# Kernel tuning notes

Hardware: AMD Instinct MI355X
Metric: run time of the kernel (lower is better)

## Reference

```python
import jax, jax.numpy as jnp
import numpy as np

B, S, XDIM, YDIM = 64, 1024, 256, 128


def setup_inputs() -> dict:
    key = jax.random.key(0)
    ks = jax.random.split(key, 7)
    q = jax.random.normal(ks[0], (B, S, XDIM), dtype=jnp.float32)
    # Linear weights in torch layout [out, in]; biases [out]
    sc = 1.0 / np.sqrt(XDIM)
    Wq = jax.random.normal(ks[1], (YDIM, XDIM), dtype=jnp.float32) * sc
    Wk = jax.random.normal(ks[2], (YDIM, XDIM), dtype=jnp.float32) * sc
    Wv = jax.random.normal(ks[3], (YDIM, XDIM), dtype=jnp.float32) * sc
    bq = jax.random.normal(ks[4], (YDIM,), dtype=jnp.float32) * sc
    bk = jax.random.normal(ks[5], (YDIM,), dtype=jnp.float32) * sc
    bv = jax.random.normal(ks[6], (YDIM,), dtype=jnp.float32) * sc
    return {"q": q, "Wq": Wq, "bq": bq, "Wk": Wk, "bk": bk, "Wv": Wv, "bv": bv}


def reference(q, Wq, bq, Wk, bk, Wv, bv):
    # Q, K, V projections: [B, S, YDIM]
    Q = jnp.einsum('bsx,yx->bsy', q, Wq) + bq
    K = jnp.einsum('bsx,yx->bsy', q, Wk) + bk
    V = jnp.einsum('bsx,yx->bsy', q, Wv) + bv
    scale = jnp.float32(np.sqrt(YDIM))
    # scores [B, S_q, S_k]; softmax over the QUERY axis (dim=-2), non-standard
    scores = jnp.einsum('bqd,bkd->bqk', Q, K) / scale
    attn = jax.nn.softmax(scores, axis=-2)
    out = jnp.einsum('bqk,bkd->bqd', attn, V)  # [B, S, YDIM]
    # flat=True: max over dim=-2 -> [B, YDIM]
    return jnp.max(out, axis=-2)
```

## Files before the change

### kernel.cpp

```cpp
#include <hip/hip_runtime.h>

typedef __bf16 bf16;
typedef __attribute__((ext_vector_type(8))) __bf16 bf16x8;
typedef __attribute__((ext_vector_type(4))) __bf16 bf16x4;
typedef __attribute__((ext_vector_type(4))) float  f32x4;

static __device__ __forceinline__ f32x4 mfma16(bf16x8 a, bf16x8 b, f32x4 c) {
  return __builtin_amdgcn_mfma_f32_16x16x32_bf16(a, b, c, 0, 0, 0);
}
static __device__ __forceinline__ float fexp2(float x) {
  return __builtin_amdgcn_exp2f(x);
}
static __device__ __forceinline__ float flog2(float x) {
  return __builtin_amdgcn_logf(x);
}

#define EXP_C1 (1.4426950408889634f / 11.313708498984760f)

typedef const __attribute__((address_space(1))) unsigned int gas_u32;
typedef __attribute__((address_space(3))) unsigned int las_u32;
#define GLDS16(gp, lp) __builtin_amdgcn_global_load_lds((gas_u32*)(gp), (las_u32*)(lp), 16, 0, 0)

#define DMA_FENCE() __asm__ volatile("s_waitcnt vmcnt(0)" ::: "memory")


__global__ __launch_bounds__(256) void k_prep(
    const float* __restrict__ Wq, const float* __restrict__ Wk,
    const float* __restrict__ Wv, bf16* __restrict__ Wc)
{
  int id = blockIdx.x * 256 + threadIdx.x;
  int proj = id >> 12, r = id & 4095;
  int g = r >> 7, n = r & 127;
  const float* W = proj == 0 ? Wq : proj == 1 ? Wk : Wv;
  const float sc = (proj == 0) ? EXP_C1 : 1.0f;
  const float4* src = (const float4*)(W + n * 256 + g * 8);
  float4 a = src[0], b = src[1];
  bf16x8 o = { (bf16)(a.x * sc), (bf16)(a.y * sc), (bf16)(a.z * sc), (bf16)(a.w * sc),
               (bf16)(b.x * sc), (bf16)(b.y * sc), (bf16)(b.z * sc), (bf16)(b.w * sc) };
  *(bf16x8*)(Wc + (size_t)proj * 32768 + g * 1024 + n * 8) = o;
}

__global__ __launch_bounds__(256, 4) void k_qkv(
    const float* __restrict__ q, const bf16* __restrict__ Wc,
    const float* __restrict__ bq, const float* __restrict__ bk, const float* __restrict__ bv,
    bf16* __restrict__ Qb, bf16* __restrict__ Kb, bf16* __restrict__ VT)
{
  __shared__ bf16 Al[32 * 520];

  const int tid = threadIdx.x, lane = tid & 63, wave = tid >> 6;
  const int ln = lane & 15, quad = lane >> 4;
  const int wc = wave;
  const int m0 = blockIdx.x * 64;

  {
    const float* src = q + (size_t)m0 * 256;
    for (int it = 0; it < 16; ++it) {
      int f = it * 1024 + tid * 4;
      int r = f >> 8, c = f & 255;
      float4 v = *(const float4*)(src + f);
      bf16x4 o = { (bf16)v.x, (bf16)v.y, (bf16)v.z, (bf16)v.w };
      *(bf16x4*)&Al[(c >> 3) * 520 + r * 8 + (c & 7)] = o;
    }
  }
  __syncthreads();

  const int b = m0 >> 10, st = (m0 & 1023) >> 7, s_off = m0 & 64;
  const size_t tbase = ((size_t)b * 8 + st) * 16384;

  for (int p = 0; p < 3; ++p) {
    const bf16* W = Wc + (size_t)p * 32768;
    const float* bias = p == 0 ? bq : p == 1 ? bk : bv;
    if (p < 2) {
      f32x4 acc[2][4] = {};
      for (int kk = 0; kk < 8; ++kk) {
        int g = kk * 4 + quad;
        bf16x8 ax[4], bw[2];
        for (int t = 0; t < 4; ++t)
          ax[t] = *(const bf16x8*)&Al[g * 520 + (t * 16 + ln) * 8];
        for (int t = 0; t < 2; ++t)
          bw[t] = *(const bf16x8*)(W + g * 1024 + (wc * 32 + t * 16 + ln) * 8);
        for (int i = 0; i < 2; ++i)
          for (int j = 0; j < 4; ++j)
            acc[i][j] = mfma16(bw[i], ax[j], acc[i][j]);
      }
      bf16* dst = (p == 0 ? Qb : Kb) + tbase;
      for (int i = 0; i < 2; ++i) {
        float4 b4 = *(const float4*)&bias[wc * 32 + i * 16 + quad * 4];
        if (p == 0) { b4.x *= EXP_C1; b4.y *= EXP_C1; b4.z *= EXP_C1; b4.w *= EXP_C1; }
        int gd = wc * 4 + i * 2 + (quad >> 1);
        int e0 = (quad & 1) * 4;
        for (int j = 0; j < 4; ++j) {
          int s = s_off + j * 16 + ln;
          bf16x4 o = { (bf16)(acc[i][j][0] + b4.x), (bf16)(acc[i][j][1] + b4.y),
                       (bf16)(acc[i][j][2] + b4.z), (bf16)(acc[i][j][3] + b4.w) };
          *(bf16x4*)&dst[(size_t)gd * 1024 + (size_t)s * 8 + e0] = o;
        }
      }
    } else {
      f32x4 acc[4][2] = {};
      for (int kk = 0; kk < 8; ++kk) {
        int g = kk * 4 + quad;
        bf16x8 ax[4], bw[2];
        for (int t = 0; t < 4; ++t)
          ax[t] = *(const bf16x8*)&Al[g * 520 + (t * 16 + ln) * 8];
        for (int t = 0; t < 2; ++t)
          bw[t] = *(const bf16x8*)(W + g * 1024 + (wc * 32 + t * 16 + ln) * 8);
        for (int i = 0; i < 4; ++i)
          for (int j = 0; j < 2; ++j)
            acc[i][j] = mfma16(ax[i], bw[j], acc[i][j]);
      }
      bf16* dst = VT + tbase;
      for (int j = 0; j < 2; ++j) {
        int d = wc * 32 + j * 16 + ln;
        float bb = bias[d];
        for (int i = 0; i < 4; ++i) {
          int s0 = s_off + i * 16 + quad * 4;
          int G  = (s0 >> 5) * 4 + ((s0 & 15) >> 2);
          int e0 = (s0 & 16) >> 2;
          bf16x4 o = { (bf16)(acc[i][j][0] + bb), (bf16)(acc[i][j][1] + bb),
                       (bf16)(acc[i][j][2] + bb), (bf16)(acc[i][j][3] + bb) };
          *(bf16x4*)&dst[(size_t)G * 1024 + (size_t)d * 8 + e0] = o;
        }
      }
    }
  }
}

__global__ __launch_bounds__(256, 2) void k_stats(
    const bf16* __restrict__ Qb, const bf16* __restrict__ Kb, float* __restrict__ nlg)
{
  __shared__ char Qbuf[2][32768];
  const int b = blockIdx.x, kt = blockIdx.y;
  const int tid = threadIdx.x, lane = tid & 63, wave = tid >> 6;
  const int ln = lane & 15, quad = lane >> 4;

  const bf16* ktile = Kb + ((size_t)b * 8 + kt) * 16384;
  bf16x8 ak[2][4];
  for (int i = 0; i < 2; ++i)
    for (int kk = 0; kk < 4; ++kk)
      ak[i][kk] = *(const bf16x8*)(ktile + (kk * 4 + quad) * 1024 + (wave * 32 + i * 16 + ln) * 8);

  const char* qb_b = (const char*)(Qb + (size_t)b * 8 * 16384);
  for (int c = 0; c < 8; ++c)
    GLDS16(qb_b + (wave * 8 + c) * 1024 + lane * 16, &Qbuf[0][(wave * 8 + c) * 1024]);

  f32x4 csum[2] = {};
  for (int qt = 0; qt < 8; ++qt) {
    DMA_FENCE();
    __syncthreads();
    if (qt < 7)
      for (int c = 0; c < 8; ++c)
        GLDS16(qb_b + (size_t)(qt + 1) * 32768 + (wave * 8 + c) * 1024 + lane * 16,
               &Qbuf[(qt + 1) & 1][(wave * 8 + c) * 1024]);
    const char* Ql = Qbuf[qt & 1];
    for (int jq = 0; jq < 8; ++jq) {
      f32x4 s0 = {}, s1 = {};
      __builtin_amdgcn_s_setprio(1);
      for (int kk = 0; kk < 4; ++kk) {
        bf16x8 bqf = *(const bf16x8*)(Ql + ((kk * 4 + quad) * 2 + (jq >> 2)) * 1024
                                         + ((jq * 16 + ln) & 63) * 16);
        s0 = mfma16(ak[0][kk], bqf, s0);
        s1 = mfma16(ak[1][kk], bqf, s1);
      }
      __builtin_amdgcn_s_setprio(0);
      for (int rr = 0; rr < 4; ++rr) {
        csum[0][rr] += fexp2(s0[rr]);
        csum[1][rr] += fexp2(s1[rr]);
      }
    }
  }
  for (int i = 0; i < 2; ++i)
    for (int rr = 0; rr < 4; ++rr) {
      float v = csum[i][rr];
      v += __shfl_xor(v, 1, 64); v += __shfl_xor(v, 2, 64);
      v += __shfl_xor(v, 4, 64); v += __shfl_xor(v, 8, 64);
      csum[i][rr] = v;
    }
  if (ln == 0) {
    float* dst = nlg + (size_t)b * 1024 + kt * 128 + wave * 32 + quad * 4;
    for (int i = 0; i < 2; ++i)
      for (int rr = 0; rr < 4; ++rr)
        dst[i * 16 + rr] = -flog2(csum[i][rr]);
  }
}

__global__ __launch_bounds__(256, 2) void k_attn(
    const bf16* __restrict__ Qb, const bf16* __restrict__ Kb, const bf16* __restrict__ VT,
    const float* __restrict__ nlg, float* __restrict__ Opart)
{
  __shared__ char buf[2][32768];
  __shared__ float nll[1024];
  __shared__ float redm[4][128];

  const int b = blockIdx.x, qt = blockIdx.y;
  const int tid = threadIdx.x, lane = tid & 63, wave = tid >> 6;
  const int ln = lane & 15, quad = lane >> 4;

  *(float4*)&nll[tid * 4] = *(const float4*)(nlg + (size_t)b * 1024 + tid * 4);

  const bf16* qtile = Qb + ((size_t)b * 8 + qt) * 16384;
  bf16x8 bq_[2][4];
  for (int j = 0; j < 2; ++j)
    for (int kk = 0; kk < 4; ++kk)
      bq_[j][kk] = *(const bf16x8*)(qtile + (kk * 4 + quad) * 1024 + (wave * 32 + j * 16 + ln) * 8);

  const char* kb_b = (const char*)(Kb + (size_t)b * 8 * 16384);
  const char* vt_b = (const char*)(VT + (size_t)b * 8 * 16384);

#define DMA_TILE(t) do {                                                         \
    const char* ksrc = kb_b + (size_t)((t) >> 1) * 32768 + ((t) & 1) * 1024;     \
    const char* vsrc = vt_b + (size_t)((t) >> 1) * 32768 + ((t) & 1) * 16384;    \
    char* d_ = buf[(t) & 1];                                                     \
    for (int c = 0; c < 4; ++c) {                                                \
      int ch = wave * 4 + c;                                                     \
      GLDS16(ksrc + ch * 2048 + lane * 16, d_ + ch * 1024);                      \
      GLDS16(vsrc + (ch >> 1) * 2048 + (ch & 1) * 1024 + lane * 16,              \
             d_ + 16384 + ch * 1024);                                            \
    }                                                                            \
  } while (0)

  f32x4 oacc[2][8] = {};
  DMA_TILE(0);

  for (int t = 0; t < 16; ++t) {
    DMA_FENCE();
    __syncthreads();
    if (t < 15) DMA_TILE(t + 1);
    const char* Kl = buf[t & 1];
    const char* Vl = buf[t & 1] + 16384;

    f32x4 sacc[4][2];
    for (int i = 0; i < 4; ++i) {
      float4 L4 = *(float4*)&nll[t * 64 + i * 16 + quad * 4];
      f32x4 ini = { L4.x, L4.y, L4.z, L4.w };
      sacc[i][0] = ini; sacc[i][1] = ini;
    }
    __builtin_amdgcn_s_setprio(1);
    for (int kk = 0; kk < 4; ++kk) {
      bf16x8 ak[4];
      for (int i = 0; i < 4; ++i)
        ak[i] = *(const bf16x8*)(Kl + (kk * 4 + quad) * 1024 + (i * 16 + ln) * 16);
      for (int i = 0; i < 4; ++i)
        for (int j = 0; j < 2; ++j)
          sacc[i][j] = mfma16(ak[i], bq_[j][kk], sacc[i][j]);
    }
    __builtin_amdgcn_s_setprio(0);
    bf16x8 pf[2][2];
    for (int s = 0; s < 2; ++s) {
      for (int j = 0; j < 2; ++j) {
        f32x4 lo = sacc[2 * s][j], hi = sacc[2 * s + 1][j];
        pf[j][s] = bf16x8{
          (bf16)fexp2(lo[0]), (bf16)fexp2(lo[1]), (bf16)fexp2(lo[2]), (bf16)fexp2(lo[3]),
          (bf16)fexp2(hi[0]), (bf16)fexp2(hi[1]), (bf16)fexp2(hi[2]), (bf16)fexp2(hi[3]) };
      }
    }
    __builtin_amdgcn_s_setprio(1);
    for (int s = 0; s < 2; ++s)
      for (int j2 = 0; j2 < 8; ++j2) {
        bf16x8 bv_ = *(const bf16x8*)(Vl + ((s * 4 + quad) * 2 + (j2 >> 2)) * 1024
                                         + ((j2 * 16 + ln) & 63) * 16);
        oacc[0][j2] = mfma16(pf[0][s], bv_, oacc[0][j2]);
        oacc[1][j2] = mfma16(pf[1][s], bv_, oacc[1][j2]);
      }
    __builtin_amdgcn_s_setprio(0);
  }
#undef DMA_TILE

  for (int j2 = 0; j2 < 8; ++j2) {
    float m = -3.4e38f;
    for (int j = 0; j < 2; ++j)
      for (int rr = 0; rr < 4; ++rr)
        m = fmaxf(m, oacc[j][j2][rr]);
    m = fmaxf(m, __shfl_xor(m, 16, 64));
    m = fmaxf(m, __shfl_xor(m, 32, 64));
    if (lane < 16) redm[wave][j2 * 16 + ln] = m;
  }
  __syncthreads();
  if (tid < 128)
    Opart[((size_t)b * 8 + qt) * 128 + tid] =
      fmaxf(fmaxf(redm[0][tid], redm[1][tid]), fmaxf(redm[2][tid], redm[3][tid]));
}

__global__ __launch_bounds__(256) void k_final(
    const float* __restrict__ Opart, float* __restrict__ out)
{
  int t = blockIdx.x * 256 + threadIdx.x;
  int b = t >> 7, d = t & 127;
  const float* p = Opart + (size_t)b * 1024 + d;
  float m = p[0];
  for (int i = 1; i < 8; ++i) m = fmaxf(m, p[(size_t)i * 128]);
  out[t] = m;
}

extern "C" void kernel_launch(void* const* d_in, const int* in_sizes, int n_in,
                              void* d_out, int out_size, void* d_ws, size_t ws_size,
                              hipStream_t stream) {
  const float* q  = (const float*)d_in[0];
  const float* Wq = (const float*)d_in[1];
  const float* bq = (const float*)d_in[2];
  const float* Wk = (const float*)d_in[3];
  const float* bk = (const float*)d_in[4];
  const float* Wv = (const float*)d_in[5];
  const float* bv = (const float*)d_in[6];
  float* out = (float*)d_out;

  char* ws = (char*)d_ws;
  bf16*  Qb    = (bf16*)(ws);
  bf16*  Kb    = (bf16*)(ws + (16u << 20));
  bf16*  VT    = (bf16*)(ws + (32u << 20));
  float* nlg   = (float*)(ws + (48u << 20));
  float* Opart = (float*)(ws + (48u << 20) + (512u << 10));
  bf16*  Wc    = (bf16*)(ws + (49u << 20));

  k_prep <<<48,           256, 0, stream>>>(Wq, Wk, Wv, Wc);
  k_qkv  <<<dim3(1024),   256, 0, stream>>>(q, Wc, bq, bk, bv, Qb, Kb, VT);
  k_stats<<<dim3(64, 8),  256, 0, stream>>>(Qb, Kb, nlg);
  k_attn <<<dim3(64, 8),  256, 0, stream>>>(Qb, Kb, VT, nlg, Opart);
  k_final<<<32, 256, 0, stream>>>(Opart, out);
}
```

Baseline: 89.37 us.

## Restructure QKV projection: 512-thread blocks, two tiles each, prefetched input, fused Q/K/V loop

The QKV projection kernel now runs 256 blocks of 512 threads, each processing two 128-row tiles instead of one 64-row tile. The next tile's fp32 input is prefetched into registers while the current one is computed, and the Q, K and V MFMA accumulations share one k-loop so each LDS A-fragment load is reused across all three projections. The aim is to hide global load latency and cut redundant LDS reads and block launches, at the cost of much higher register pressure (the prefetch buffer plus three accumulator sets) and fewer blocks in flight.

```diff
diff --git a/kernel.cpp b/kernel.cpp
--- a/kernel.cpp
+++ b/kernel.cpp
@@ -40,85 +40,109 @@
   *(bf16x8*)(Wc + (size_t)proj * 32768 + g * 1024 + n * 8) = o;
 }
 
-__global__ __launch_bounds__(256, 4) void k_qkv(
+__global__ __launch_bounds__(512, 2) void k_qkv(
     const float* __restrict__ q, const bf16* __restrict__ Wc,
     const float* __restrict__ bq, const float* __restrict__ bk, const float* __restrict__ bv,
     bf16* __restrict__ Qb, bf16* __restrict__ Kb, bf16* __restrict__ VT)
 {
-  __shared__ bf16 Al[32 * 520];
+  __shared__ bf16 Al[32 * 1032];
 
   const int tid = threadIdx.x, lane = tid & 63, wave = tid >> 6;
   const int ln = lane & 15, quad = lane >> 4;
-  const int wc = wave;
-  const int m0 = blockIdx.x * 64;
-
+  const int wr = wave >> 2, wc = wave & 3;
+  const int tile0 = blockIdx.x * 2;
+
+  float4 pre[16];
   {
-    const float* src = q + (size_t)m0 * 256;
-    for (int it = 0; it < 16; ++it) {
-      int f = it * 1024 + tid * 4;
+    const float* src = q + (size_t)tile0 * 32768;
+    #pragma unroll
+    for (int i = 0; i < 16; ++i) pre[i] = *(const float4*)(src + i * 2048 + tid * 4);
+  }
+
+  for (int it = 0; it < 2; ++it) {
+    __syncthreads();
+    #pragma unroll
+    for (int i = 0; i < 16; ++i) {
+      int f = i * 2048 + tid * 4;
       int r = f >> 8, c = f & 255;
-      float4 v = *(const float4*)(src + f);
+      float4 v = pre[i];
       bf16x4 o = { (bf16)v.x, (bf16)v.y, (bf16)v.z, (bf16)v.w };
-      *(bf16x4*)&Al[(c >> 3) * 520 + r * 8 + (c & 7)] = o;
-    }
-  }
-  __syncthreads();
-
-  const int b = m0 >> 10, st = (m0 & 1023) >> 7, s_off = m0 & 64;
-  const size_t tbase = ((size_t)b * 8 + st) * 16384;
-
-  for (int p = 0; p < 3; ++p) {
-    const bf16* W = Wc + (size_t)p * 32768;
-    const float* bias = p == 0 ? bq : p == 1 ? bk : bv;
-    if (p < 2) {
-      f32x4 acc[2][4] = {};
-      for (int kk = 0; kk < 8; ++kk) {
-        int g = kk * 4 + quad;
-        bf16x8 ax[4], bw[2];
-        for (int t = 0; t < 4; ++t)
-          ax[t] = *(const bf16x8*)&Al[g * 520 + (t * 16 + ln) * 8];
-        for (int t = 0; t < 2; ++t)
-          bw[t] = *(const bf16x8*)(W + g * 1024 + (wc * 32 + t * 16 + ln) * 8);
-        for (int i = 0; i < 2; ++i)
-          for (int j = 0; j < 4; ++j)
-            acc[i][j] = mfma16(bw[i], ax[j], acc[i][j]);
-      }
+      *(bf16x4*)&Al[(c >> 3) * 1032 + r * 8 + (c & 7)] = o;
+    }
+    __syncthreads();
+    if (it < 1) {
+      const float* src = q + (size_t)(tile0 + 1) * 32768;
+      #pragma unroll
+      for (int i = 0; i < 16; ++i) pre[i] = *(const float4*)(src + i * 2048 + tid * 4);
+    }
+
+    const int m0 = (tile0 + it) * 128;
+    const int b = m0 >> 10, st = (m0 >> 7) & 7;
+    const size_t tbase = ((size_t)b * 8 + st) * 16384;
+
+    f32x4 aQ[2][4] = {}, aK[2][4] = {}, aV[4][2] = {};
+    for (int kk = 0; kk < 8; ++kk) {
+      int g = kk * 4 + quad;
+      bf16x8 ax[4];
+      #pragma unroll
+      for (int t = 0; t < 4; ++t)
+        ax[t] = *(const bf16x8*)&Al[g * 1032 + (wr * 64 + t * 16 + ln) * 8];
+      bf16x8 bwQ[2], bwK[2], bwV[2];
+      #pragma unroll
+      for (int t = 0; t < 2; ++t) {
+        const int off = g * 1024 + (wc * 32 + t * 16 + ln) * 8;
+        bwQ[t] = *(const bf16x8*)(Wc + off);
+        bwK[t] = *(const bf16x8*)(Wc + 32768 + off);
+        bwV[t] = *(const bf16x8*)(Wc + 65536 + off);
+      }
+      __builtin_amdgcn_s_setprio(1);
+      #pragma unroll
+      for (int i = 0; i < 2; ++i)
+        #pragma unroll
+        for (int j = 0; j < 4; ++j) {
+          aQ[i][j] = mfma16(bwQ[i], ax[j], aQ[i][j]);
+          aK[i][j] = mfma16(bwK[i], ax[j], aK[i][j]);
+        }
+      #pragma unroll
+      for (int i = 0; i < 4; ++i)
+        #pragma unroll
+        for (int j = 0; j < 2; ++j)
+          aV[i][j] = mfma16(ax[i], bwV[j], aV[i][j]);
+      __builtin_amdgcn_s_setprio(0);
+    }
+
+    for (int p = 0; p < 2; ++p) {
       bf16* dst = (p == 0 ? Qb : Kb) + tbase;
+      const float* bias = p == 0 ? bq : bk;
+      #pragma unroll
       for (int i = 0; i < 2; ++i) {
         float4 b4 = *(const float4*)&bias[wc * 32 + i * 16 + quad * 4];
         if (p == 0) { b4.x *= EXP_C1; b4.y *= EXP_C1; b4.z *= EXP_C1; b4.w *= EXP_C1; }
         int gd = wc * 4 + i * 2 + (quad >> 1);
         int e0 = (quad & 1) * 4;
+        #pragma unroll
         for (int j = 0; j < 4; ++j) {
-          int s = s_off + j * 16 + ln;
-          bf16x4 o = { (bf16)(acc[i][j][0] + b4.x), (bf16)(acc[i][j][1] + b4.y),
-                       (bf16)(acc[i][j][2] + b4.z), (bf16)(acc[i][j][3] + b4.w) };
+          int s = wr * 64 + j * 16 + ln;
+          const f32x4 a_ = p == 0 ? aQ[i][j] : aK[i][j];
+          bf16x4 o = { (bf16)(a_[0] + b4.x), (bf16)(a_[1] + b4.y),
+                       (bf16)(a_[2] + b4.z), (bf16)(a_[3] + b4.w) };
           *(bf16x4*)&dst[(size_t)gd * 1024 + (size_t)s * 8 + e0] = o;
         }
       }
-    } else {
-      f32x4 acc[4][2] = {};
-      for (int kk = 0; kk < 8; ++kk) {
-        int g = kk * 4 + quad;
-        bf16x8 ax[4], bw[2];
-        for (int t = 0; t < 4; ++t)
-          ax[t] = *(const bf16x8*)&Al[g * 520 + (t * 16 + ln) * 8];
-        for (int t = 0; t < 2; ++t)
-          bw[t] = *(const bf16x8*)(W + g * 1024 + (wc * 32 + t * 16 + ln) * 8);
-        for (int i = 0; i < 4; ++i)
-          for (int j = 0; j < 2; ++j)
-            acc[i][j] = mfma16(ax[i], bw[j], acc[i][j]);
-      }
+    }
+    {
       bf16* dst = VT + tbase;
+      #pragma unroll
       for (int j = 0; j < 2; ++j) {
         int d = wc * 32 + j * 16 + ln;
-        float bb = bias[d];
+        float bb = bv[d];
+        #pragma unroll
         for (int i = 0; i < 4; ++i) {
-          int s0 = s_off + i * 16 + quad * 4;
+          int s0 = wr * 64 + i * 16 + quad * 4;
           int G  = (s0 >> 5) * 4 + ((s0 & 15) >> 2);
           int e0 = (s0 & 16) >> 2;
-          bf16x4 o = { (bf16)(acc[i][j][0] + bb), (bf16)(acc[i][j][1] + bb),
-                       (bf16)(acc[i][j][2] + bb), (bf16)(acc[i][j][3] + bb) };
+          bf16x4 o = { (bf16)(aV[i][j][0] + bb), (bf16)(aV[i][j][1] + bb),
+                       (bf16)(aV[i][j][2] + bb), (bf16)(aV[i][j][3] + bb) };
           *(bf16x4*)&dst[(size_t)G * 1024 + (size_t)d * 8 + e0] = o;
         }
       }
@@ -313,7 +337,7 @@
   bf16*  Wc    = (bf16*)(ws + (49u << 20));
 
   k_prep <<<48,           256, 0, stream>>>(Wq, Wk, Wv, Wc);
-  k_qkv  <<<dim3(1024),   256, 0, stream>>>(q, Wc, bq, bk, bv, Qb, Kb, VT);
+  k_qkv  <<<dim3(256),    512, 0, stream>>>(q, Wc, bq, bk, bv, Qb, Kb, VT);
   k_stats<<<dim3(64, 8),  256, 0, stream>>>(Qb, Kb, nlg);
   k_attn <<<dim3(64, 8),  256, 0, stream>>>(Qb, Kb, VT, nlg, Opart);
   k_final<<<32, 256, 0, stream>>>(Opart, out);
```

Result: slower. 161.3 us (+80.5%).

## Fuse final max into attention via float atomics and prefetch QKV weights

Applied to the files above, without the earlier changes.

Drops the k_final launch. k_prep now initializes the output to -inf, and each k_attn block merges its partial column max into the output with integer atomicMax/atomicMin on the float bit patterns. Separately, the QKV projection kernel software-pipelines the weight fragment loads four k-steps ahead and fully unrolls its loops. The atomic trick depends on sign-split int/uint ordering and on k_prep running before k_attn. The prefetch adds register pressure under the launch bound of 4.

```diff
diff --git a/kernel.cpp b/kernel.cpp
--- a/kernel.cpp
+++ b/kernel.cpp
@@ -26,9 +26,10 @@
 
 __global__ __launch_bounds__(256) void k_prep(
     const float* __restrict__ Wq, const float* __restrict__ Wk,
-    const float* __restrict__ Wv, bf16* __restrict__ Wc)
+    const float* __restrict__ Wv, bf16* __restrict__ Wc, float* __restrict__ out)
 {
   int id = blockIdx.x * 256 + threadIdx.x;
+  if (id < 8192) out[id] = -__builtin_inff();
   int proj = id >> 12, r = id & 4095;
   int g = r >> 7, n = r & 127;
   const float* W = proj == 0 ? Wq : proj == 1 ? Wk : Wv;
@@ -54,6 +55,7 @@
 
   {
     const float* src = q + (size_t)m0 * 256;
+    #pragma unroll
     for (int it = 0; it < 16; ++it) {
       int f = it * 1024 + tid * 4;
       int r = f >> 8, c = f & 255;
@@ -67,28 +69,43 @@
   const int b = m0 >> 10, st = (m0 & 1023) >> 7, s_off = m0 & 64;
   const size_t tbase = ((size_t)b * 8 + st) * 16384;
 
+#define BW_LOAD(slot, kkv) do {                                                  \
+    bwp[slot][0] = *(const bf16x8*)(W + ((kkv) * 4 + quad) * 1024 + (wc * 32 + ln) * 8);        \
+    bwp[slot][1] = *(const bf16x8*)(W + ((kkv) * 4 + quad) * 1024 + (wc * 32 + 16 + ln) * 8);   \
+  } while (0)
+
   for (int p = 0; p < 3; ++p) {
     const bf16* W = Wc + (size_t)p * 32768;
     const float* bias = p == 0 ? bq : p == 1 ? bk : bv;
+    bf16x8 bwp[4][2];
+    #pragma unroll
+    for (int k2 = 0; k2 < 4; ++k2) BW_LOAD(k2, k2);
+
     if (p < 2) {
       f32x4 acc[2][4] = {};
+      #pragma unroll
       for (int kk = 0; kk < 8; ++kk) {
         int g = kk * 4 + quad;
-        bf16x8 ax[4], bw[2];
+        bf16x8 ax[4];
+        #pragma unroll
         for (int t = 0; t < 4; ++t)
           ax[t] = *(const bf16x8*)&Al[g * 520 + (t * 16 + ln) * 8];
-        for (int t = 0; t < 2; ++t)
-          bw[t] = *(const bf16x8*)(W + g * 1024 + (wc * 32 + t * 16 + ln) * 8);
-        for (int i = 0; i < 2; ++i)
-          for (int j = 0; j < 4; ++j)
-            acc[i][j] = mfma16(bw[i], ax[j], acc[i][j]);
+        bf16x8 b0 = bwp[kk & 3][0], b1 = bwp[kk & 3][1];
+        if (kk < 4) BW_LOAD(kk & 3, kk + 4);
+        #pragma unroll
+        for (int j = 0; j < 4; ++j) {
+          acc[0][j] = mfma16(b0, ax[j], acc[0][j]);
+          acc[1][j] = mfma16(b1, ax[j], acc[1][j]);
+        }
       }
       bf16* dst = (p == 0 ? Qb : Kb) + tbase;
+      #pragma unroll
       for (int i = 0; i < 2; ++i) {
         float4 b4 = *(const float4*)&bias[wc * 32 + i * 16 + quad * 4];
         if (p == 0) { b4.x *= EXP_C1; b4.y *= EXP_C1; b4.z *= EXP_C1; b4.w *= EXP_C1; }
         int gd = wc * 4 + i * 2 + (quad >> 1);
         int e0 = (quad & 1) * 4;
+        #pragma unroll
         for (int j = 0; j < 4; ++j) {
           int s = s_off + j * 16 + ln;
           bf16x4 o = { (bf16)(acc[i][j][0] + b4.x), (bf16)(acc[i][j][1] + b4.y),
@@ -98,21 +115,27 @@
       }
     } else {
       f32x4 acc[4][2] = {};
+      #pragma unroll
       for (int kk = 0; kk < 8; ++kk) {
         int g = kk * 4 + quad;
-        bf16x8 ax[4], bw[2];
+        bf16x8 ax[4];
+        #pragma unroll
         for (int t = 0; t < 4; ++t)
           ax[t] = *(const bf16x8*)&Al[g * 520 + (t * 16 + ln) * 8];
-        for (int t = 0; t < 2; ++t)
-          bw[t] = *(const bf16x8*)(W + g * 1024 + (wc * 32 + t * 16 + ln) * 8);
-        for (int i = 0; i < 4; ++i)
-          for (int j = 0; j < 2; ++j)
-            acc[i][j] = mfma16(ax[i], bw[j], acc[i][j]);
+        bf16x8 b0 = bwp[kk & 3][0], b1 = bwp[kk & 3][1];
+        if (kk < 4) BW_LOAD(kk & 3, kk + 4);
+        #pragma unroll
+        for (int i = 0; i < 4; ++i) {
+          acc[i][0] = mfma16(ax[i], b0, acc[i][0]);
+          acc[i][1] = mfma16(ax[i], b1, acc[i][1]);
+        }
       }
       bf16* dst = VT + tbase;
+      #pragma unroll
       for (int j = 0; j < 2; ++j) {
         int d = wc * 32 + j * 16 + ln;
         float bb = bias[d];
+        #pragma unroll
         for (int i = 0; i < 4; ++i) {
           int s0 = s_off + i * 16 + quad * 4;
           int G  = (s0 >> 5) * 4 + ((s0 & 15) >> 2);
@@ -124,6 +147,7 @@
       }
     }
   }
+#undef BW_LOAD
 }
 
 __global__ __launch_bounds__(256, 2) void k_stats(
@@ -186,7 +210,7 @@
 
 __global__ __launch_bounds__(256, 2) void k_attn(
     const bf16* __restrict__ Qb, const bf16* __restrict__ Kb, const bf16* __restrict__ VT,
-    const float* __restrict__ nlg, float* __restrict__ Opart)
+    const float* __restrict__ nlg, float* __restrict__ out)
 {
   __shared__ char buf[2][32768];
   __shared__ float nll[1024];
@@ -276,20 +300,12 @@
     if (lane < 16) redm[wave][j2 * 16 + ln] = m;
   }
   __syncthreads();
-  if (tid < 128)
-    Opart[((size_t)b * 8 + qt) * 128 + tid] =
-      fmaxf(fmaxf(redm[0][tid], redm[1][tid]), fmaxf(redm[2][tid], redm[3][tid]));
-}
-
-__global__ __launch_bounds__(256) void k_final(
-    const float* __restrict__ Opart, float* __restrict__ out)
-{
-  int t = blockIdx.x * 256 + threadIdx.x;
-  int b = t >> 7, d = t & 127;
-  const float* p = Opart + (size_t)b * 1024 + d;
-  float m = p[0];
-  for (int i = 1; i < 8; ++i) m = fmaxf(m, p[(size_t)i * 128]);
-  out[t] = m;
+  if (tid < 128) {
+    float m = fmaxf(fmaxf(redm[0][tid], redm[1][tid]), fmaxf(redm[2][tid], redm[3][tid]));
+    float* addr = out + (size_t)b * 128 + tid;
+    if (m >= 0.0f) atomicMax((int*)addr, __float_as_int(m));
+    else           atomicMin((unsigned int*)addr, __float_as_uint(m));
+  }
 }
 
 extern "C" void kernel_launch(void* const* d_in, const int* in_sizes, int n_in,
@@ -309,12 +325,10 @@
   bf16*  Kb    = (bf16*)(ws + (16u << 20));
   bf16*  VT    = (bf16*)(ws + (32u << 20));
   float* nlg   = (float*)(ws + (48u << 20));
-  float* Opart = (float*)(ws + (48u << 20) + (512u << 10));
   bf16*  Wc    = (bf16*)(ws + (49u << 20));
 
-  k_prep <<<48,           256, 0, stream>>>(Wq, Wk, Wv, Wc);
+  k_prep <<<48,           256, 0, stream>>>(Wq, Wk, Wv, Wc, out);
   k_qkv  <<<dim3(1024),   256, 0, stream>>>(q, Wc, bq, bk, bv, Qb, Kb, VT);
   k_stats<<<dim3(64, 8),  256, 0, stream>>>(Qb, Kb, nlg);
-  k_attn <<<dim3(64, 8),  256, 0, stream>>>(Qb, Kb, VT, nlg, Opart);
-  k_final<<<32, 256, 0, stream>>>(Opart, out);
-}
+  k_attn <<<dim3(64, 8),  256, 0, stream>>>(Qb, Kb, VT, nlg, out);
+}
```

New measurement: 87.94 us. No clear change (-1.6%).
